# Performance work log

Measured on AMD Instinct MI355X. Metric: run time of the kernel, lower is better.

The kernel has to match this reference:

```python
import jax, jax.numpy as jnp
import numpy as np
from jax import lax

# ---- static config (matches init_kwargs) ----
BATCH, SEQ, D_MODEL = 2, 512, 1024
D_STATE, EXPAND, HEADDIM, D_CONV = 64, 2, 64, 4
VNUM, HORIZON = 3, 20
D_INNER = EXPAND * D_MODEL            # 2048
NHEADS = D_INNER // HEADDIM           # 32
CONV_DIM = D_INNER + 2 * D_STATE      # x, B, C go through the depthwise conv
D_IN_PROJ = 2 * D_INNER + 2 * D_STATE + NHEADS  # z | xBC | dt
RMS_EPS = 1e-5


def setup_inputs() -> dict:
    key = jax.random.key(0)
    ks = jax.random.split(key, 10)
    s = 0.02
    return {
        "embed_data": jax.random.normal(ks[0], (BATCH, SEQ, D_MODEL), jnp.float32),
        "in_proj_w": (jax.random.normal(ks[1], (D_IN_PROJ, D_MODEL), jnp.float32) * s),
        "conv_w": (jax.random.normal(ks[2], (CONV_DIM, D_CONV), jnp.float32) * s),
        "conv_b": jnp.zeros((CONV_DIM,), jnp.float32),
        # dt_bias = softplus^{-1}(dt_init) with dt_init ~ U(1e-3, 0.1), as in Mamba2
        "dt_bias": jnp.log(jnp.expm1(jax.random.uniform(ks[3], (NHEADS,), jnp.float32, 1e-3, 0.1))),
        # A = -exp(A_log), A_init ~ U(1, 16)
        "A_log": jnp.log(jax.random.uniform(ks[4], (NHEADS,), jnp.float32, 1.0, 16.0)),
        "D": jnp.ones((NHEADS,), jnp.float32),
        "norm_w": jnp.ones((D_INNER,), jnp.float32),
        "out_proj_w": (jax.random.normal(ks[5], (D_MODEL, D_INNER), jnp.float32) * s),
        "dec_cur_w": (jax.random.normal(ks[6], (VNUM, D_MODEL), jnp.float32) * s),
        "dec_cur_b": jnp.zeros((VNUM,), jnp.float32),
        "dec_fut_w": (jax.random.normal(ks[7], (HORIZON * VNUM, D_MODEL), jnp.float32) * s),
        "dec_fut_b": jnp.zeros((HORIZON * VNUM,), jnp.float32),
    }


def _mamba2(embed_data, in_proj_w, conv_w, conv_b, dt_bias, A_log, D, norm_w, out_proj_w):
    b, s, _ = embed_data.shape
    zxbcdt = jnp.einsum('bsd,ed->bse', embed_data, in_proj_w)  # [B,S,D_IN_PROJ]
    z = zxbcdt[..., :D_INNER]
    xBC = zxbcdt[..., D_INNER:D_INNER + CONV_DIM]
    dt = zxbcdt[..., D_INNER + CONV_DIM:]                      # [B,S,H]

    # causal depthwise conv1d (kernel=4) + silu
    xpad = jnp.pad(xBC, ((0, 0), (D_CONV - 1, 0), (0, 0)))
    xBC = sum(conv_w[:, k] * xpad[:, k:k + s, :] for k in range(D_CONV)) + conv_b
    xBC = jax.nn.silu(xBC)

    x = xBC[..., :D_INNER].reshape(b, s, NHEADS, HEADDIM)       # [B,S,H,P]
    Bm = xBC[..., D_INNER:D_INNER + D_STATE]                    # [B,S,N]
    Cm = xBC[..., D_INNER + D_STATE:]                           # [B,S,N]

    dt = jax.nn.softplus(dt + dt_bias)                          # [B,S,H]
    A = -jnp.exp(A_log)                                         # [H]

    # selective state-space scan: h_t = exp(dt*A) h_{t-1} + dt * x_t B_t^T
    def step(h, inp):
        x_t, dt_t, b_t, c_t = inp                               # [B,H,P],[B,H],[B,N],[B,N]
        dA = jnp.exp(dt_t * A)                                  # [B,H]
        h = h * dA[..., None, None] + (dt_t[..., None] * x_t)[..., None] * b_t[:, None, None, :]
        y = jnp.einsum('bhpn,bn->bhp', h, c_t)
        return h, y

    h0 = jnp.zeros((b, NHEADS, HEADDIM, D_STATE), embed_data.dtype)
    xs = (x.transpose(1, 0, 2, 3), dt.transpose(1, 0, 2),
          Bm.transpose(1, 0, 2), Cm.transpose(1, 0, 2))
    _, ys = lax.scan(step, h0, xs)                              # [S,B,H,P]
    y = ys.transpose(1, 0, 2, 3) + D[None, None, :, None] * x   # skip term D*x
    y = y.reshape(b, s, D_INNER)

    # gated RMSNorm: rmsnorm(y * silu(z)) * w
    y = y * jax.nn.silu(z)
    y = y * lax.rsqrt(jnp.mean(y * y, axis=-1, keepdims=True) + RMS_EPS) * norm_w
    return jnp.einsum('bsi,di->bsd', y, out_proj_w)             # [B,S,D_MODEL]


def reference(embed_data, in_proj_w, conv_w, conv_b, dt_bias, A_log, D, norm_w,
              out_proj_w, dec_cur_w, dec_cur_b, dec_fut_w, dec_fut_b):
    h = _mamba2(embed_data, in_proj_w, conv_w, conv_b, dt_bias, A_log, D, norm_w, out_proj_w)
    pred_current = jnp.einsum('bsd,vd->bsv', h, dec_cur_w) + dec_cur_b         # [B,S,V]
    pred_future = (h[:, -1] @ dec_fut_w.T + dec_fut_b).reshape(h.shape[0], HORIZON, VNUM)
    return (pred_current, pred_future)
```

## Files before the change

kernel.cpp:

```cpp
#include <hip/hip_runtime.h>
#include <hip/hip_bf16.h>

#define BATCH   2
#define SEQ     512
#define DMODEL  1024
#define DSTATE  64
#define HEADDIM 64
#define DCONV   4
#define VNUM    3
#define HORIZON 20
#define DINNER  2048
#define NHEADS  32
#define CONVDIM 2176
#define DINPROJ 4256
#define NPAD1   4352
#define BS      (BATCH*SEQ)
#define RMS_EPS 1e-5f
#define CHUNK   64
#define NCHUNK  (SEQ/CHUNK)
#define NDEC    (VNUM + HORIZON*VNUM)
#define WC_DS   32

typedef __attribute__((ext_vector_type(8))) short bf16x8;
typedef __attribute__((ext_vector_type(4))) float f32x4;

__device__ __forceinline__ unsigned short f2b(float x) {
    union { float f; unsigned u; } v; v.f = x;
    return (unsigned short)((v.u + 0x7fffu + ((v.u >> 16) & 1u)) >> 16);
}

__device__ __forceinline__ void async16(const void* g, const void* l) {
    __builtin_amdgcn_global_load_lds(
        (const __attribute__((address_space(1))) unsigned int*)g,
        (__attribute__((address_space(3))) unsigned int*)l, 16, 0, 0);
}

template<int BM, int BN, int FM, int FN, int KD>
__global__ __launch_bounds__(256) void gemm_bf16(const short* __restrict__ A,
                                                 const short* __restrict__ B,
                                                 float* __restrict__ C, int N) {
    constexpr int WM = FM * 16, WN = FN * 16;
    static_assert(BM == 2 * WM && BN == 2 * WN, "2x2 waves");
    __shared__ __align__(16) short At[BM * 32];
    __shared__ __align__(16) short Bt[BN * 32];
    const int t    = threadIdx.x;
    const int lane = t & 63;
    const int w    = t >> 6;
    const int wm   = (w >> 1) * WM, wn = (w & 1) * WN;
    const int row0 = blockIdx.y * BM, col0 = blockIdx.x * BN;
    const int fr   = lane & 15;
    const int kq   = lane >> 4;
    const int lr   = t >> 2;
    const int lc   = (t & 3) * 8;

    const short* Ag = A + (size_t)(row0 + lr) * KD + lc;
    const short* Bg = B + (size_t)(col0 + lr) * KD + lc;

    f32x4 acc[FM][FN];
#pragma unroll
    for (int i = 0; i < FM; ++i)
#pragma unroll
        for (int j = 0; j < FN; ++j)
#pragma unroll
            for (int r = 0; r < 4; ++r) acc[i][j][r] = 0.f;

    for (int k0 = 0; k0 < KD; k0 += 32) {
        __syncthreads();
#pragma unroll
        for (int i = 0; i < BM / 64; ++i)
            async16(Ag + (size_t)i * 64 * KD + k0, (const char*)At + i * 4096 + t * 16);
#pragma unroll
        for (int i = 0; i < BN / 64; ++i)
            async16(Bg + (size_t)i * 64 * KD + k0, (const char*)Bt + i * 4096 + t * 16);
        __syncthreads();

        bf16x8 af[FM], bv[FN];
#pragma unroll
        for (int i = 0; i < FM; ++i)
            af[i] = *(const bf16x8*)&At[(wm + i * 16 + fr) * 32 + kq * 8];
#pragma unroll
        for (int j = 0; j < FN; ++j)
            bv[j] = *(const bf16x8*)&Bt[(wn + j * 16 + fr) * 32 + kq * 8];
#pragma unroll
        for (int i = 0; i < FM; ++i)
#pragma unroll
            for (int j = 0; j < FN; ++j)
                acc[i][j] = __builtin_amdgcn_mfma_f32_16x16x32_bf16(
                    af[i], bv[j], acc[i][j], 0, 0, 0);
    }

    const int orow = lane >> 4;
#pragma unroll
    for (int i = 0; i < FM; ++i)
#pragma unroll
        for (int j = 0; j < FN; ++j) {
            const int col = col0 + wn + j * 16 + fr;
            if (col < N) {
#pragma unroll
                for (int r = 0; r < 4; ++r) {
                    const int row = row0 + wm + i * 16 + orow * 4 + r;
                    C[(size_t)row * N + col] = acc[i][j][r];
                }
            }
        }
}

#define EMB4  (BS * DMODEL / 4)
#define IPW4  (NPAD1 * DMODEL / 4)
__global__ __launch_bounds__(256) void cast_fused_kernel(
        const float* __restrict__ embed, const float* __restrict__ ipw,
        short* __restrict__ embB, short* __restrict__ ipwB) {
    const int i = blockIdx.x * 256 + threadIdx.x;
    if (i < EMB4) {
        float4 v = *(const float4*)(embed + (size_t)i * 4);
        *(short4*)(embB + (size_t)i * 4) =
            make_short4((short)f2b(v.x), (short)f2b(v.y),
                        (short)f2b(v.z), (short)f2b(v.w));
    } else {
        const int j = i - EMB4;
        const size_t e0 = (size_t)j * 4;
        const int row = (int)(e0 / DMODEL);
        short4 o;
        if (row < DINPROJ) {
            float4 v = *(const float4*)(ipw + e0);
            o = make_short4((short)f2b(v.x), (short)f2b(v.y),
                            (short)f2b(v.z), (short)f2b(v.w));
        } else {
            o = make_short4(0, 0, 0, 0);
        }
        *(short4*)(ipwB + e0) = o;
    }
}

__global__ __launch_bounds__(256) void wcomb_partial_kernel(
        const float* __restrict__ op, const float* __restrict__ cw,
        const float* __restrict__ fw, float* __restrict__ P) {
    const int itile = blockIdx.x & 7;
    const int ds    = blockIdx.x >> 3;
    const int i     = itile * 256 + threadIdx.x;
    const int d0    = ds * 32;

    __shared__ float lw[32][64];
#pragma unroll
    for (int k = 0; k < 8; ++k) {
        const int e = threadIdx.x * 8 + k;
        const int d = e >> 6, v = e & 63;
        float val = 0.f;
        if (v < VNUM)      val = cw[(size_t)v * DMODEL + d0 + d];
        else if (v < NDEC) val = fw[(size_t)(v - VNUM) * DMODEL + d0 + d];
        lw[d][v] = val;
    }

    float opc[32];
#pragma unroll
    for (int d = 0; d < 32; ++d) opc[d] = op[(size_t)(d0 + d) * DINNER + i];
    __syncthreads();

    f32x4 acc[16];
#pragma unroll
    for (int q = 0; q < 16; ++q)
#pragma unroll
        for (int r = 0; r < 4; ++r) acc[q][r] = 0.f;

#pragma unroll
    for (int d = 0; d < 32; ++d) {
        const float o = opc[d];
#pragma unroll
        for (int q = 0; q < 16; ++q) {
            float4 wv = *(const float4*)&lw[d][q * 4];
            acc[q][0] += o * wv.x; acc[q][1] += o * wv.y;
            acc[q][2] += o * wv.z; acc[q][3] += o * wv.w;
        }
    }

    float* Pp = P + (size_t)ds * 64 * DINNER + i;
#pragma unroll
    for (int q = 0; q < 16; ++q)
#pragma unroll
        for (int r = 0; r < 4; ++r)
            Pp[(size_t)(q * 4 + r) * DINNER] = acc[q][r];
}

__global__ __launch_bounds__(256) void wcomb_reduce_kernel(
        const float* __restrict__ P, float* __restrict__ W) {
    const int idx = blockIdx.x * 256 + threadIdx.x;
    float s = 0.f;
#pragma unroll
    for (int ds = 0; ds < WC_DS; ++ds) s += P[(size_t)ds * 64 * DINNER + idx];
    W[idx] = s;
}

#define CONVBLKS (BS * CONVDIM / 4 / 256)
__global__ __launch_bounds__(256) void conv_dt_kernel(
        const float* __restrict__ zxbcdt, const float* __restrict__ cw,
        const float* __restrict__ cb, const float* __restrict__ dt_bias,
        float* __restrict__ xbc, float* __restrict__ dts) {
    if (blockIdx.x < CONVBLKS) {
        const int item = blockIdx.x * 256 + threadIdx.x;
        const int c4 = item % (CONVDIM / 4);
        const int rs = item / (CONVDIM / 4);
        const int s  = rs % SEQ;
        const int c  = c4 * 4;
        const float* src = zxbcdt + (size_t)rs * DINPROJ + DINNER + c;
        float4 x0 = (s >= 3) ? *(const float4*)(src - 3 * DINPROJ) : make_float4(0,0,0,0);
        float4 x1 = (s >= 2) ? *(const float4*)(src - 2 * DINPROJ) : make_float4(0,0,0,0);
        float4 x2 = (s >= 1) ? *(const float4*)(src - 1 * DINPROJ) : make_float4(0,0,0,0);
        float4 x3 = *(const float4*)(src);
        float4 bias = *(const float4*)(cb + c);
        float4 r;
        {
            float4 w = *(const float4*)(cw + (size_t)(c+0)*4);
            r.x = bias.x + w.x*x0.x + w.y*x1.x + w.z*x2.x + w.w*x3.x;
        }
        {
            float4 w = *(const float4*)(cw + (size_t)(c+1)*4);
            r.y = bias.y + w.x*x0.y + w.y*x1.y + w.z*x2.y + w.w*x3.y;
        }
        {
            float4 w = *(const float4*)(cw + (size_t)(c+2)*4);
            r.z = bias.z + w.x*x0.z + w.y*x1.z + w.z*x2.z + w.w*x3.z;
        }
        {
            float4 w = *(const float4*)(cw + (size_t)(c+3)*4);
            r.w = bias.w + w.x*x0.w + w.y*x1.w + w.z*x2.w + w.w*x3.w;
        }
        r.x = r.x / (1.f + expf(-r.x));
        r.y = r.y / (1.f + expf(-r.y));
        r.z = r.z / (1.f + expf(-r.z));
        r.w = r.w / (1.f + expf(-r.w));
        *(float4*)(xbc + (size_t)rs * CONVDIM + c) = r;
    } else {
        const int idx = (blockIdx.x - CONVBLKS) * 256 + threadIdx.x;
        if (idx < BS * NHEADS) {
            const int h  = idx % NHEADS;
            const int rs = idx / NHEADS;
            const float v = zxbcdt[(size_t)rs * DINPROJ + DINNER + CONVDIM + h]
                            + dt_bias[h];
            dts[idx] = fmaxf(v, 0.f) + log1pf(expf(-fabsf(v)));
        }
    }
}

__global__ __launch_bounds__(256) void chunk_intra_kernel(
        const float* __restrict__ xbc, const float* __restrict__ dts,
        const float* __restrict__ A_log, const float* __restrict__ Dv,
        float* __restrict__ yraw, float* __restrict__ Sc,
        float* __restrict__ dexp) {
    const int blk = blockIdx.x;
    const int c  = blk & 7;
    const int bh = blk >> 3;
    const int h  = bh & 31;
    const int b  = bh >> 5;
    const int rs0 = b * SEQ + c * CHUNK;

    __shared__ float sBn[64][68];
    __shared__ float sX [64][68];
    __shared__ float sMT[64][68];
    __shared__ float sl[64], se[64], sdt[64];

    const int tid = threadIdx.x;
    const float A = -expf(A_log[h]);

    {
        const int row = tid >> 2;
        const int cq  = tid & 3;
        const float* xrow = xbc + (size_t)(rs0 + row) * CONVDIM;
#pragma unroll
        for (int i = 0; i < 4; ++i) {
            const int n = cq * 16 + i * 4;
            float4 bv = *(const float4*)(xrow + DINNER + n);
            float4 cv = *(const float4*)(xrow + DINNER + DSTATE + n);
            sBn[n+0][row] = bv.x; sBn[n+1][row] = bv.y;
            sBn[n+2][row] = bv.z; sBn[n+3][row] = bv.w;
            sX [n+0][row] = cv.x; sX [n+1][row] = cv.y;
            sX [n+2][row] = cv.z; sX [n+3][row] = cv.w;
        }
    }

    if (tid < 64) {
        const float dtv = dts[(size_t)(rs0 + tid) * NHEADS + h];
        sdt[tid] = dtv;
        float v = dtv * A;
#pragma unroll
        for (int off = 1; off < 64; off <<= 1) {
            float o = __shfl_up(v, off, 64);
            if (tid >= off) v += o;
        }
        sl[tid] = v;
        const float ltot = __shfl(v, 63, 64);
        se[tid] = expf(ltot - v);
        dexp[(size_t)blk * 64 + tid] = expf(v);
    }
    __syncthreads();

    const int g0 = (tid >> 4) * 4;
    const int g1 = (tid & 15) * 4;

    {
        const int t0 = g0, s0 = g1;
        float acc[4][4] = {};
        for (int n = 0; n < 64; ++n) {
            float4 ct = *(const float4*)&sX [n][t0];
            float4 bs = *(const float4*)&sBn[n][s0];
            float cta[4] = {ct.x, ct.y, ct.z, ct.w};
            float bsa[4] = {bs.x, bs.y, bs.z, bs.w};
#pragma unroll
            for (int i = 0; i < 4; ++i)
#pragma unroll
                for (int j = 0; j < 4; ++j) acc[i][j] += cta[i] * bsa[j];
        }
#pragma unroll
        for (int i = 0; i < 4; ++i) {
            const int t = t0 + i;
            const float lt = sl[t];
#pragma unroll
            for (int j = 0; j < 4; ++j) {
                const int s = s0 + j;
                sMT[s][t] = (s <= t) ? expf(lt - sl[s]) * acc[i][j] : 0.f;
            }
        }
    }
    __syncthreads();

    {
        const int row = tid >> 2;
        const int cq  = tid & 3;
        const float* xrow = xbc + (size_t)(rs0 + row) * CONVDIM + h * HEADDIM;
        const float dtv = sdt[row];
#pragma unroll
        for (int i = 0; i < 4; ++i) {
            const int p = cq * 16 + i * 4;
            float4 xv = *(const float4*)(xrow + p);
            sX[row][p+0] = dtv * xv.x; sX[row][p+1] = dtv * xv.y;
            sX[row][p+2] = dtv * xv.z; sX[row][p+3] = dtv * xv.w;
        }
    }
    __syncthreads();

    {
        const int t0 = g0, p0 = g1;
        float acc[4][4] = {};
        for (int s = 0; s < 64; ++s) {
            float4 mt = *(const float4*)&sMT[s][t0];
            float4 us = *(const float4*)&sX [s][p0];
            float mta[4] = {mt.x, mt.y, mt.z, mt.w};
            float usa[4] = {us.x, us.y, us.z, us.w};
#pragma unroll
            for (int i = 0; i < 4; ++i)
#pragma unroll
                for (int j = 0; j < 4; ++j) acc[i][j] += mta[i] * usa[j];
        }
        const float Dh = Dv[h];
#pragma unroll
        for (int i = 0; i < 4; ++i) {
            const int t = t0 + i;
            float4 xv = *(const float4*)(xbc + (size_t)(rs0 + t) * CONVDIM
                                         + h * HEADDIM + p0);
            float4 yv = make_float4(acc[i][0] + Dh * xv.x, acc[i][1] + Dh * xv.y,
                                    acc[i][2] + Dh * xv.z, acc[i][3] + Dh * xv.w);
            *(float4*)&yraw[(size_t)(rs0 + t) * DINNER + h * HEADDIM + p0] = yv;
        }
    }

    {
        const int p0 = g0, n0 = g1;
        float acc[4][4] = {};
        for (int s = 0; s < 64; ++s) {
            const float es = se[s];
            float4 up = *(const float4*)&sX[s][p0];
            float upa[4] = {es * up.x, es * up.y, es * up.z, es * up.w};
            float bna[4] = {sBn[n0+0][s], sBn[n0+1][s], sBn[n0+2][s], sBn[n0+3][s]};
#pragma unroll
            for (int i = 0; i < 4; ++i)
#pragma unroll
                for (int j = 0; j < 4; ++j) acc[i][j] += upa[i] * bna[j];
        }
        float* scp = Sc + (size_t)blk * (HEADDIM * DSTATE);
#pragma unroll
        for (int i = 0; i < 4; ++i) {
            float4 v = make_float4(acc[i][0], acc[i][1], acc[i][2], acc[i][3]);
            *(float4*)&scp[(size_t)(p0 + i) * DSTATE + n0] = v;
        }
    }
}

__global__ __launch_bounds__(256) void state_combine_kernel(
        const float* __restrict__ Sc, const float* __restrict__ dexp,
        float* __restrict__ h0ws) {
    const int bh  = blockIdx.x;
    const int tid = threadIdx.x;
    float hreg[16];
#pragma unroll
    for (int k = 0; k < 16; ++k) hreg[k] = 0.f;
    for (int c = 0; c < NCHUNK; ++c) {
        const size_t base = (size_t)(bh * NCHUNK + c) * (HEADDIM * DSTATE);
        const float ac = dexp[(size_t)(bh * NCHUNK + c) * 64 + 63];
#pragma unroll
        for (int k = 0; k < 16; ++k) {
            const int e = tid + k * 256;
            h0ws[base + e] = hreg[k];
            hreg[k] = ac * hreg[k] + Sc[base + e];
        }
    }
}

__global__ __launch_bounds__(256) void chunk_state_out_kernel(
        const float* __restrict__ xbc, const float* __restrict__ h0ws,
        const float* __restrict__ dexp, float* __restrict__ yraw) {
    const int blk = blockIdx.x;
    const int c  = blk & 7;
    if (c == 0) return;
    const int bh = blk >> 3;
    const int h  = bh & 31;
    const int b  = bh >> 5;
    const int rs0 = b * SEQ + c * CHUNK;

    __shared__ float sCn[64][68];
    __shared__ float sH [64][68];
    __shared__ float sdex[64];
    const int tid = threadIdx.x;
    {
        const int row = tid >> 2;
        const int cq  = tid & 3;
        const float* xrow = xbc + (size_t)(rs0 + row) * CONVDIM + DINNER + DSTATE;
        const float* hrow = h0ws + (size_t)blk * (HEADDIM * DSTATE) + (size_t)row * DSTATE;
#pragma unroll
        for (int i = 0; i < 4; ++i) {
            const int n = cq * 16 + i * 4;
            float4 cv = *(const float4*)(xrow + n);
            float4 hv = *(const float4*)(hrow + n);
            sCn[n+0][row] = cv.x; sCn[n+1][row] = cv.y;
            sCn[n+2][row] = cv.z; sCn[n+3][row] = cv.w;
            sH [n+0][row] = hv.x; sH [n+1][row] = hv.y;
            sH [n+2][row] = hv.z; sH [n+3][row] = hv.w;
        }
    }
    if (tid < 64) sdex[tid] = dexp[(size_t)blk * 64 + tid];
    __syncthreads();

    const int t0 = (tid >> 4) * 4;
    const int p0 = (tid & 15) * 4;
    float acc[4][4] = {};
    for (int n = 0; n < 64; ++n) {
        float4 ct = *(const float4*)&sCn[n][t0];
        float4 hp = *(const float4*)&sH [n][p0];
        float cta[4] = {ct.x, ct.y, ct.z, ct.w};
        float hpa[4] = {hp.x, hp.y, hp.z, hp.w};
#pragma unroll
        for (int i = 0; i < 4; ++i)
#pragma unroll
            for (int j = 0; j < 4; ++j) acc[i][j] += cta[i] * hpa[j];
    }
#pragma unroll
    for (int i = 0; i < 4; ++i) {
        const float d = sdex[t0 + i];
        float* yp = &yraw[(size_t)(rs0 + t0 + i) * DINNER + h * HEADDIM + p0];
        float4 old = *(const float4*)yp;
        *(float4*)yp = make_float4(old.x + d * acc[i][0], old.y + d * acc[i][1],
                                   old.z + d * acc[i][2], old.w + d * acc[i][3]);
    }
}

__global__ __launch_bounds__(256) void gate_norm_pred_kernel(
        const float* __restrict__ zxbcdt, const float* __restrict__ y,
        const float* __restrict__ nw, const float* __restrict__ W,
        const float* __restrict__ cur_b, float* __restrict__ out,
        float* __restrict__ ylast) {
    const int rs = blockIdx.x;
    const int t  = threadIdx.x;
    const float* z  = zxbcdt + (size_t)rs * DINPROJ;
    const float* yr = y + (size_t)rs * DINNER;

    float vals[8];
    float ss = 0.f;
#pragma unroll
    for (int i = 0; i < 8; ++i) {
        const int c = t + i * 256;
        const float zv = z[c];
        const float v  = yr[c] * (zv / (1.f + expf(-zv)));
        vals[i] = v;
        ss += v * v;
    }
#pragma unroll
    for (int off = 32; off > 0; off >>= 1) ss += __shfl_down(ss, off, 64);
    __shared__ float red[4];
    if ((t & 63) == 0) red[t >> 6] = ss;
    __syncthreads();
    const float tot   = red[0] + red[1] + red[2] + red[3];
    const float scale = rsqrtf(tot / (float)DINNER + RMS_EPS);

    const bool is_last = ((rs & (SEQ - 1)) == SEQ - 1);
    float p0 = 0.f, p1 = 0.f, p2 = 0.f;
#pragma unroll
    for (int i = 0; i < 8; ++i) {
        const int c = t + i * 256;
        const float vn = vals[i] * scale * nw[c];
        vals[i] = vn;
        p0 += vn * W[c];
        p1 += vn * W[DINNER + c];
        p2 += vn * W[2 * DINNER + c];
    }
    if (is_last) {
        float* yl = ylast + (size_t)(rs >> 9) * DINNER;
#pragma unroll
        for (int i = 0; i < 8; ++i) yl[t + i * 256] = vals[i];
    }
#pragma unroll
    for (int off = 32; off > 0; off >>= 1) {
        p0 += __shfl_down(p0, off, 64);
        p1 += __shfl_down(p1, off, 64);
        p2 += __shfl_down(p2, off, 64);
    }
    __shared__ float r3[4][3];
    if ((t & 63) == 0) { r3[t >> 6][0] = p0; r3[t >> 6][1] = p1; r3[t >> 6][2] = p2; }
    __syncthreads();
    if (t < VNUM) {
        const float s = r3[0][t] + r3[1][t] + r3[2][t] + r3[3][t];
        out[(size_t)rs * VNUM + t] = s + cur_b[t];
    }
}

__global__ __launch_bounds__(256) void pred_fut_kernel(
        const float* __restrict__ ylast, const float* __restrict__ W,
        const float* __restrict__ bvec, float* __restrict__ out) {
    const int blk = blockIdx.x;
    const int b = blk / (HORIZON * VNUM);
    const int j = blk % (HORIZON * VNUM);
    const float* yl = ylast + (size_t)b * DINNER;
    const float* wr = W + (size_t)(VNUM + j) * DINNER;
    float pv = 0.f;
    for (int i = threadIdx.x; i < DINNER; i += 256) pv += yl[i] * wr[i];
#pragma unroll
    for (int off = 32; off > 0; off >>= 1) pv += __shfl_down(pv, off, 64);
    __shared__ float red[4];
    if ((threadIdx.x & 63) == 0) red[threadIdx.x >> 6] = pv;
    __syncthreads();
    if (threadIdx.x == 0)
        out[b * (HORIZON * VNUM) + j] = red[0] + red[1] + red[2] + red[3] + bvec[j];
}

extern "C" void kernel_launch(void* const* d_in, const int* in_sizes, int n_in,
                              void* d_out, int out_size, void* d_ws, size_t ws_size,
                              hipStream_t stream) {
    const float* embed      = (const float*)d_in[0];
    const float* in_proj_w  = (const float*)d_in[1];
    const float* conv_w     = (const float*)d_in[2];
    const float* conv_b     = (const float*)d_in[3];
    const float* dt_bias    = (const float*)d_in[4];
    const float* A_log      = (const float*)d_in[5];
    const float* Dv         = (const float*)d_in[6];
    const float* norm_w     = (const float*)d_in[7];
    const float* out_proj_w = (const float*)d_in[8];
    const float* dec_cur_w  = (const float*)d_in[9];
    const float* dec_cur_b  = (const float*)d_in[10];
    const float* dec_fut_w  = (const float*)d_in[11];
    const float* dec_fut_b  = (const float*)d_in[12];

    float* ws     = (float*)d_ws;
    float* zxbcdt = ws;
    float* xbc    = zxbcdt + (size_t)BS * DINPROJ;
    float* dts    = xbc    + (size_t)BS * CONVDIM;
    float* yraw   = dts    + (size_t)BS * NHEADS;
    float* Sc     = yraw   + (size_t)BS * DINNER;
    float* h0ws   = Sc     + (size_t)BATCH*NHEADS*NCHUNK*HEADDIM*DSTATE;
    float* dexp   = h0ws   + (size_t)BATCH*NHEADS*NCHUNK*HEADDIM*DSTATE;
    float* Wp     = dexp   + (size_t)BATCH*NHEADS*NCHUNK*64;
    float* W      = Wp     + (size_t)WC_DS * 64 * DINNER;
    float* ylast  = W      + (size_t)64 * DINNER;
    short* embB   = (short*)(ylast + (size_t)BATCH * DINNER);
    short* ipwB   = embB + (size_t)BS * DMODEL;

    float* out = (float*)d_out;

    wcomb_partial_kernel<<<8 * WC_DS, 256, 0, stream>>>(out_proj_w, dec_cur_w,
                                                        dec_fut_w, Wp);
    wcomb_reduce_kernel<<<64 * DINNER / 256, 256, 0, stream>>>(Wp, W);

    cast_fused_kernel<<<(EMB4 + IPW4) / 256, 256, 0, stream>>>(embed, in_proj_w, embB, ipwB);
    gemm_bf16<128, 64, 4, 2, DMODEL>
        <<<dim3(NPAD1 / 64, BS / 128), 256, 0, stream>>>(embB, ipwB, zxbcdt, DINPROJ);

    conv_dt_kernel<<<CONVBLKS + (BS * NHEADS + 255) / 256, 256, 0, stream>>>(
        zxbcdt, conv_w, conv_b, dt_bias, xbc, dts);

    chunk_intra_kernel<<<BATCH * NHEADS * NCHUNK, 256, 0, stream>>>(
        xbc, dts, A_log, Dv, yraw, Sc, dexp);
    state_combine_kernel<<<BATCH * NHEADS, 256, 0, stream>>>(Sc, dexp, h0ws);
    chunk_state_out_kernel<<<BATCH * NHEADS * NCHUNK, 256, 0, stream>>>(
        xbc, h0ws, dexp, yraw);

    gate_norm_pred_kernel<<<BS, 256, 0, stream>>>(zxbcdt, yraw, norm_w, W,
                                                  dec_cur_b, out, ylast);

    pred_fut_kernel<<<BATCH * HORIZON * VNUM, 256, 0, stream>>>(ylast, W, dec_fut_b,
                                                                out + BS * VNUM);
}
```

Measured before the change: 186.9 us.

## Fuse conv and dt into chunk kernels and merge small preprocessing launches

The standalone conv/dt kernel and its xbc/dts intermediate buffers are removed. The chunk kernels now recompute the causal depthwise conv, SiLU and softplus directly from the in_proj output. The D skip term is rebuilt from the dt-scaled x kept in shared memory, by dividing by dt. The bf16 cast is merged with the wcomb partial kernel, and the wcomb reduce is merged with a state-combine pass that now splits work across 4x more blocks. This cuts launches and global traffic, at the cost of recomputing the B/C conv once per head and per chunk kernel.

```diff
diff --git a/kernel.cpp b/kernel.cpp
--- a/kernel.cpp
+++ b/kernel.cpp
@@ -29,6 +29,8 @@
     return (unsigned short)((v.u + 0x7fffu + ((v.u >> 16) & 1u)) >> 16);
 }
 
+__device__ __forceinline__ float silu(float x) { return x / (1.f + expf(-x)); }
+
 __device__ __forceinline__ void async16(const void* g, const void* l) {
     __builtin_amdgcn_global_load_lds(
         (const __attribute__((address_space(1))) unsigned int*)g,
@@ -105,49 +107,51 @@
         }
 }
 
-#define EMB4  (BS * DMODEL / 4)
-#define IPW4  (NPAD1 * DMODEL / 4)
-__global__ __launch_bounds__(256) void cast_fused_kernel(
+#define EMB4     (BS * DMODEL / 4)
+#define IPW4     (NPAD1 * DMODEL / 4)
+#define CASTBLKS ((EMB4 + IPW4) / 256)
+__global__ __launch_bounds__(256) void prep_kernel(
         const float* __restrict__ embed, const float* __restrict__ ipw,
-        short* __restrict__ embB, short* __restrict__ ipwB) {
-    const int i = blockIdx.x * 256 + threadIdx.x;
-    if (i < EMB4) {
-        float4 v = *(const float4*)(embed + (size_t)i * 4);
-        *(short4*)(embB + (size_t)i * 4) =
-            make_short4((short)f2b(v.x), (short)f2b(v.y),
-                        (short)f2b(v.z), (short)f2b(v.w));
-    } else {
-        const int j = i - EMB4;
-        const size_t e0 = (size_t)j * 4;
-        const int row = (int)(e0 / DMODEL);
-        short4 o;
-        if (row < DINPROJ) {
-            float4 v = *(const float4*)(ipw + e0);
-            o = make_short4((short)f2b(v.x), (short)f2b(v.y),
+        short* __restrict__ embB, short* __restrict__ ipwB,
+        const float* __restrict__ op, const float* __restrict__ cwv,
+        const float* __restrict__ fwv, float* __restrict__ P) {
+    __shared__ float lw[32][64];
+    if (blockIdx.x < CASTBLKS) {
+        const int i = blockIdx.x * 256 + threadIdx.x;
+        if (i < EMB4) {
+            float4 v = *(const float4*)(embed + (size_t)i * 4);
+            *(short4*)(embB + (size_t)i * 4) =
+                make_short4((short)f2b(v.x), (short)f2b(v.y),
                             (short)f2b(v.z), (short)f2b(v.w));
         } else {
-            o = make_short4(0, 0, 0, 0);
-        }
-        *(short4*)(ipwB + e0) = o;
-    }
-}
-
-__global__ __launch_bounds__(256) void wcomb_partial_kernel(
-        const float* __restrict__ op, const float* __restrict__ cw,
-        const float* __restrict__ fw, float* __restrict__ P) {
-    const int itile = blockIdx.x & 7;
-    const int ds    = blockIdx.x >> 3;
+            const int j = i - EMB4;
+            const size_t e0 = (size_t)j * 4;
+            const int row = (int)(e0 / DMODEL);
+            short4 o;
+            if (row < DINPROJ) {
+                float4 v = *(const float4*)(ipw + e0);
+                o = make_short4((short)f2b(v.x), (short)f2b(v.y),
+                                (short)f2b(v.z), (short)f2b(v.w));
+            } else {
+                o = make_short4(0, 0, 0, 0);
+            }
+            *(short4*)(ipwB + e0) = o;
+        }
+        return;
+    }
+    const int blk   = blockIdx.x - CASTBLKS;
+    const int itile = blk & 7;
+    const int ds    = blk >> 3;
     const int i     = itile * 256 + threadIdx.x;
     const int d0    = ds * 32;
 
-    __shared__ float lw[32][64];
 #pragma unroll
     for (int k = 0; k < 8; ++k) {
         const int e = threadIdx.x * 8 + k;
         const int d = e >> 6, v = e & 63;
         float val = 0.f;
-        if (v < VNUM)      val = cw[(size_t)v * DMODEL + d0 + d];
-        else if (v < NDEC) val = fw[(size_t)(v - VNUM) * DMODEL + d0 + d];
+        if (v < VNUM)      val = cwv[(size_t)v * DMODEL + d0 + d];
+        else if (v < NDEC) val = fwv[(size_t)(v - VNUM) * DMODEL + d0 + d];
         lw[d][v] = val;
     }
 
@@ -181,68 +185,9 @@
             Pp[(size_t)(q * 4 + r) * DINNER] = acc[q][r];
 }
 
-__global__ __launch_bounds__(256) void wcomb_reduce_kernel(
-        const float* __restrict__ P, float* __restrict__ W) {
-    const int idx = blockIdx.x * 256 + threadIdx.x;
-    float s = 0.f;
-#pragma unroll
-    for (int ds = 0; ds < WC_DS; ++ds) s += P[(size_t)ds * 64 * DINNER + idx];
-    W[idx] = s;
-}
-
-#define CONVBLKS (BS * CONVDIM / 4 / 256)
-__global__ __launch_bounds__(256) void conv_dt_kernel(
-        const float* __restrict__ zxbcdt, const float* __restrict__ cw,
+__global__ __launch_bounds__(256) void chunk_intra_kernel(
+        const float* __restrict__ zx, const float* __restrict__ cw,
         const float* __restrict__ cb, const float* __restrict__ dt_bias,
-        float* __restrict__ xbc, float* __restrict__ dts) {
-    if (blockIdx.x < CONVBLKS) {
-        const int item = blockIdx.x * 256 + threadIdx.x;
-        const int c4 = item % (CONVDIM / 4);
-        const int rs = item / (CONVDIM / 4);
-        const int s  = rs % SEQ;
-        const int c  = c4 * 4;
-        const float* src = zxbcdt + (size_t)rs * DINPROJ + DINNER + c;
-        float4 x0 = (s >= 3) ? *(const float4*)(src - 3 * DINPROJ) : make_float4(0,0,0,0);
-        float4 x1 = (s >= 2) ? *(const float4*)(src - 2 * DINPROJ) : make_float4(0,0,0,0);
-        float4 x2 = (s >= 1) ? *(const float4*)(src - 1 * DINPROJ) : make_float4(0,0,0,0);
-        float4 x3 = *(const float4*)(src);
-        float4 bias = *(const float4*)(cb + c);
-        float4 r;
-        {
-            float4 w = *(const float4*)(cw + (size_t)(c+0)*4);
-            r.x = bias.x + w.x*x0.x + w.y*x1.x + w.z*x2.x + w.w*x3.x;
-        }
-        {
-            float4 w = *(const float4*)(cw + (size_t)(c+1)*4);
-            r.y = bias.y + w.x*x0.y + w.y*x1.y + w.z*x2.y + w.w*x3.y;
-        }
-        {
-            float4 w = *(const float4*)(cw + (size_t)(c+2)*4);
-            r.z = bias.z + w.x*x0.z + w.y*x1.z + w.z*x2.z + w.w*x3.z;
-        }
-        {
-            float4 w = *(const float4*)(cw + (size_t)(c+3)*4);
-            r.w = bias.w + w.x*x0.w + w.y*x1.w + w.z*x2.w + w.w*x3.w;
-        }
-        r.x = r.x / (1.f + expf(-r.x));
-        r.y = r.y / (1.f + expf(-r.y));
-        r.z = r.z / (1.f + expf(-r.z));
-        r.w = r.w / (1.f + expf(-r.w));
-        *(float4*)(xbc + (size_t)rs * CONVDIM + c) = r;
-    } else {
-        const int idx = (blockIdx.x - CONVBLKS) * 256 + threadIdx.x;
-        if (idx < BS * NHEADS) {
-            const int h  = idx % NHEADS;
-            const int rs = idx / NHEADS;
-            const float v = zxbcdt[(size_t)rs * DINPROJ + DINNER + CONVDIM + h]
-                            + dt_bias[h];
-            dts[idx] = fmaxf(v, 0.f) + log1pf(expf(-fabsf(v)));
-        }
-    }
-}
-
-__global__ __launch_bounds__(256) void chunk_intra_kernel(
-        const float* __restrict__ xbc, const float* __restrict__ dts,
         const float* __restrict__ A_log, const float* __restrict__ Dv,
         float* __restrict__ yraw, float* __restrict__ Sc,
         float* __restrict__ dexp) {
@@ -261,24 +206,10 @@
     const int tid = threadIdx.x;
     const float A = -expf(A_log[h]);
 
-    {
-        const int row = tid >> 2;
-        const int cq  = tid & 3;
-        const float* xrow = xbc + (size_t)(rs0 + row) * CONVDIM;
-#pragma unroll
-        for (int i = 0; i < 4; ++i) {
-            const int n = cq * 16 + i * 4;
-            float4 bv = *(const float4*)(xrow + DINNER + n);
-            float4 cv = *(const float4*)(xrow + DINNER + DSTATE + n);
-            sBn[n+0][row] = bv.x; sBn[n+1][row] = bv.y;
-            sBn[n+2][row] = bv.z; sBn[n+3][row] = bv.w;
-            sX [n+0][row] = cv.x; sX [n+1][row] = cv.y;
-            sX [n+2][row] = cv.z; sX [n+3][row] = cv.w;
-        }
-    }
-
     if (tid < 64) {
-        const float dtv = dts[(size_t)(rs0 + tid) * NHEADS + h];
+        const float raw = zx[(size_t)(rs0 + tid) * DINPROJ + DINNER + CONVDIM + h]
+                          + dt_bias[h];
+        const float dtv = fmaxf(raw, 0.f) + log1pf(expf(-fabsf(raw)));
         sdt[tid] = dtv;
         float v = dtv * A;
 #pragma unroll
@@ -290,6 +221,42 @@
         const float ltot = __shfl(v, 63, 64);
         se[tid] = expf(ltot - v);
         dexp[(size_t)blk * 64 + tid] = expf(v);
+    }
+
+    {
+        const int row  = tid >> 2;
+        const int cq   = tid & 3;
+        const int spos = c * CHUNK + row;
+        const float* src = zx + (size_t)(rs0 + row) * DINPROJ + DINNER;
+#pragma unroll
+        for (int i = 0; i < 4; ++i) {
+            const int n = cq * 16 + i * 4;
+            float tB[4][4], tC[4][4];
+#pragma unroll
+            for (int j = 0; j < 4; ++j) {
+                if (spos >= 3 - j) {
+                    const float* tr = src + (ptrdiff_t)(j - 3) * DINPROJ;
+                    float4 bv = *(const float4*)(tr + 2048 + n);
+                    float4 cv = *(const float4*)(tr + 2112 + n);
+                    tB[j][0]=bv.x; tB[j][1]=bv.y; tB[j][2]=bv.z; tB[j][3]=bv.w;
+                    tC[j][0]=cv.x; tC[j][1]=cv.y; tC[j][2]=cv.z; tC[j][3]=cv.w;
+                } else {
+#pragma unroll
+                    for (int l = 0; l < 4; ++l) { tB[j][l] = 0.f; tC[j][l] = 0.f; }
+                }
+            }
+#pragma unroll
+            for (int l = 0; l < 4; ++l) {
+                float4 wB = *(const float4*)(cw + (size_t)(2048 + n + l) * 4);
+                float4 wC = *(const float4*)(cw + (size_t)(2112 + n + l) * 4);
+                float vB = cb[2048 + n + l] + wB.x * tB[0][l] + wB.y * tB[1][l]
+                           + wB.z * tB[2][l] + wB.w * tB[3][l];
+                float vC = cb[2112 + n + l] + wC.x * tC[0][l] + wC.y * tC[1][l]
+                           + wC.z * tC[2][l] + wC.w * tC[3][l];
+                sBn[n + l][row] = silu(vB);
+                sX [n + l][row] = silu(vC);
+            }
+        }
     }
     __syncthreads();
 
@@ -323,16 +290,32 @@
     __syncthreads();
 
     {
-        const int row = tid >> 2;
-        const int cq  = tid & 3;
-        const float* xrow = xbc + (size_t)(rs0 + row) * CONVDIM + h * HEADDIM;
+        const int row  = tid >> 2;
+        const int cq   = tid & 3;
+        const int spos = c * CHUNK + row;
         const float dtv = sdt[row];
+        const float* src = zx + (size_t)(rs0 + row) * DINPROJ + DINNER + h * HEADDIM;
 #pragma unroll
         for (int i = 0; i < 4; ++i) {
             const int p = cq * 16 + i * 4;
-            float4 xv = *(const float4*)(xrow + p);
-            sX[row][p+0] = dtv * xv.x; sX[row][p+1] = dtv * xv.y;
-            sX[row][p+2] = dtv * xv.z; sX[row][p+3] = dtv * xv.w;
+            float tx[4][4];
+#pragma unroll
+            for (int j = 0; j < 4; ++j) {
+                if (spos >= 3 - j) {
+                    float4 xv = *(const float4*)(src + (ptrdiff_t)(j - 3) * DINPROJ + p);
+                    tx[j][0]=xv.x; tx[j][1]=xv.y; tx[j][2]=xv.z; tx[j][3]=xv.w;
+                } else {
+#pragma unroll
+                    for (int l = 0; l < 4; ++l) tx[j][l] = 0.f;
+                }
+            }
+#pragma unroll
+            for (int l = 0; l < 4; ++l) {
+                float4 w = *(const float4*)(cw + (size_t)(h * HEADDIM + p + l) * 4);
+                float v = cb[h * HEADDIM + p + l] + w.x * tx[0][l] + w.y * tx[1][l]
+                          + w.z * tx[2][l] + w.w * tx[3][l];
+                sX[row][p + l] = dtv * silu(v);
+            }
         }
     }
     __syncthreads();
@@ -354,10 +337,10 @@
 #pragma unroll
         for (int i = 0; i < 4; ++i) {
             const int t = t0 + i;
-            float4 xv = *(const float4*)(xbc + (size_t)(rs0 + t) * CONVDIM
-                                         + h * HEADDIM + p0);
-            float4 yv = make_float4(acc[i][0] + Dh * xv.x, acc[i][1] + Dh * xv.y,
-                                    acc[i][2] + Dh * xv.z, acc[i][3] + Dh * xv.w);
+            const float dr = Dh / sdt[t];
+            float4 uv = *(const float4*)&sX[t][p0];
+            float4 yv = make_float4(acc[i][0] + dr * uv.x, acc[i][1] + dr * uv.y,
+                                    acc[i][2] + dr * uv.z, acc[i][3] + dr * uv.w);
             *(float4*)&yraw[(size_t)(rs0 + t) * DINNER + h * HEADDIM + p0] = yv;
         }
     }
@@ -384,28 +367,34 @@
     }
 }
 
-__global__ __launch_bounds__(256) void state_combine_kernel(
+__global__ __launch_bounds__(256) void comb_reduce_kernel(
         const float* __restrict__ Sc, const float* __restrict__ dexp,
-        float* __restrict__ h0ws) {
-    const int bh  = blockIdx.x;
-    const int tid = threadIdx.x;
-    float hreg[16];
-#pragma unroll
-    for (int k = 0; k < 16; ++k) hreg[k] = 0.f;
-    for (int c = 0; c < NCHUNK; ++c) {
-        const size_t base = (size_t)(bh * NCHUNK + c) * (HEADDIM * DSTATE);
-        const float ac = dexp[(size_t)(bh * NCHUNK + c) * 64 + 63];
-#pragma unroll
-        for (int k = 0; k < 16; ++k) {
-            const int e = tid + k * 256;
-            h0ws[base + e] = hreg[k];
-            hreg[k] = ac * hreg[k] + Sc[base + e];
-        }
+        float* __restrict__ h0ws, const float* __restrict__ P,
+        float* __restrict__ W) {
+    if (blockIdx.x < 256) {
+        const int bh = blockIdx.x >> 2;
+        const int e  = (blockIdx.x & 3) * 1024 + threadIdx.x * 4;
+        float4 h = make_float4(0.f, 0.f, 0.f, 0.f);
+        for (int c = 0; c < NCHUNK; ++c) {
+            const size_t base = (size_t)(bh * NCHUNK + c) * (HEADDIM * DSTATE);
+            const float ac = dexp[(size_t)(bh * NCHUNK + c) * 64 + 63];
+            *(float4*)&h0ws[base + e] = h;
+            float4 s = *(const float4*)&Sc[base + e];
+            h.x = ac * h.x + s.x; h.y = ac * h.y + s.y;
+            h.z = ac * h.z + s.z; h.w = ac * h.w + s.w;
+        }
+    } else {
+        const int idx = (blockIdx.x - 256) * 256 + threadIdx.x;
+        float s = 0.f;
+#pragma unroll
+        for (int ds = 0; ds < WC_DS; ++ds) s += P[(size_t)ds * 64 * DINNER + idx];
+        W[idx] = s;
     }
 }
 
 __global__ __launch_bounds__(256) void chunk_state_out_kernel(
-        const float* __restrict__ xbc, const float* __restrict__ h0ws,
+        const float* __restrict__ zx, const float* __restrict__ cw,
+        const float* __restrict__ cb, const float* __restrict__ h0ws,
         const float* __restrict__ dexp, float* __restrict__ yraw) {
     const int blk = blockIdx.x;
     const int c  = blk & 7;
@@ -422,17 +411,30 @@
     {
         const int row = tid >> 2;
         const int cq  = tid & 3;
-        const float* xrow = xbc + (size_t)(rs0 + row) * CONVDIM + DINNER + DSTATE;
-        const float* hrow = h0ws + (size_t)blk * (HEADDIM * DSTATE) + (size_t)row * DSTATE;
+        const float* src  = zx + (size_t)(rs0 + row) * DINPROJ + DINNER + 2112;
+        const float* hrow = h0ws + (size_t)blk * (HEADDIM * DSTATE)
+                            + (size_t)row * DSTATE;
 #pragma unroll
         for (int i = 0; i < 4; ++i) {
             const int n = cq * 16 + i * 4;
-            float4 cv = *(const float4*)(xrow + n);
+            float4 q0 = *(const float4*)(src - 3 * DINPROJ + n);
+            float4 q1 = *(const float4*)(src - 2 * DINPROJ + n);
+            float4 q2 = *(const float4*)(src - 1 * DINPROJ + n);
+            float4 q3 = *(const float4*)(src + n);
+            float t0a[4] = {q0.x, q0.y, q0.z, q0.w};
+            float t1a[4] = {q1.x, q1.y, q1.z, q1.w};
+            float t2a[4] = {q2.x, q2.y, q2.z, q2.w};
+            float t3a[4] = {q3.x, q3.y, q3.z, q3.w};
+#pragma unroll
+            for (int l = 0; l < 4; ++l) {
+                float4 w = *(const float4*)(cw + (size_t)(2112 + n + l) * 4);
+                float v = cb[2112 + n + l] + w.x * t0a[l] + w.y * t1a[l]
+                          + w.z * t2a[l] + w.w * t3a[l];
+                sCn[n + l][row] = silu(v);
+            }
             float4 hv = *(const float4*)(hrow + n);
-            sCn[n+0][row] = cv.x; sCn[n+1][row] = cv.y;
-            sCn[n+2][row] = cv.z; sCn[n+3][row] = cv.w;
-            sH [n+0][row] = hv.x; sH [n+1][row] = hv.y;
-            sH [n+2][row] = hv.z; sH [n+3][row] = hv.w;
+            sH[n+0][row] = hv.x; sH[n+1][row] = hv.y;
+            sH[n+2][row] = hv.z; sH[n+3][row] = hv.w;
         }
     }
     if (tid < 64) sdex[tid] = dexp[(size_t)blk * 64 + tid];
@@ -558,9 +560,7 @@
 
     float* ws     = (float*)d_ws;
     float* zxbcdt = ws;
-    float* xbc    = zxbcdt + (size_t)BS * DINPROJ;
-    float* dts    = xbc    + (size_t)BS * CONVDIM;
-    float* yraw   = dts    + (size_t)BS * NHEADS;
+    float* yraw   = zxbcdt + (size_t)BS * DINPROJ;
     float* Sc     = yraw   + (size_t)BS * DINNER;
     float* h0ws   = Sc     + (size_t)BATCH*NHEADS*NCHUNK*HEADDIM*DSTATE;
     float* dexp   = h0ws   + (size_t)BATCH*NHEADS*NCHUNK*HEADDIM*DSTATE;
@@ -572,22 +572,20 @@
 
     float* out = (float*)d_out;
 
-    wcomb_partial_kernel<<<8 * WC_DS, 256, 0, stream>>>(out_proj_w, dec_cur_w,
-                                                        dec_fut_w, Wp);
-    wcomb_reduce_kernel<<<64 * DINNER / 256, 256, 0, stream>>>(Wp, W);
-
-    cast_fused_kernel<<<(EMB4 + IPW4) / 256, 256, 0, stream>>>(embed, in_proj_w, embB, ipwB);
+    prep_kernel<<<CASTBLKS + 8 * WC_DS, 256, 0, stream>>>(
+        embed, in_proj_w, embB, ipwB, out_proj_w, dec_cur_w, dec_fut_w, Wp);
+
     gemm_bf16<128, 64, 4, 2, DMODEL>
         <<<dim3(NPAD1 / 64, BS / 128), 256, 0, stream>>>(embB, ipwB, zxbcdt, DINPROJ);
 
-    conv_dt_kernel<<<CONVBLKS + (BS * NHEADS + 255) / 256, 256, 0, stream>>>(
-        zxbcdt, conv_w, conv_b, dt_bias, xbc, dts);
-
     chunk_intra_kernel<<<BATCH * NHEADS * NCHUNK, 256, 0, stream>>>(
-        xbc, dts, A_log, Dv, yraw, Sc, dexp);
-    state_combine_kernel<<<BATCH * NHEADS, 256, 0, stream>>>(Sc, dexp, h0ws);
+        zxbcdt, conv_w, conv_b, dt_bias, A_log, Dv, yraw, Sc, dexp);
+
+    comb_reduce_kernel<<<256 + 64 * DINNER / 256, 256, 0, stream>>>(
+        Sc, dexp, h0ws, Wp, W);
+
     chunk_state_out_kernel<<<BATCH * NHEADS * NCHUNK, 256, 0, stream>>>(
-        xbc, h0ws, dexp, yraw);
+        zxbcdt, conv_w, conv_b, h0ws, dexp, yraw);
 
     gate_norm_pred_kernel<<<BS, 256, 0, stream>>>(zxbcdt, yraw, norm_w, W,
                                                   dec_cur_b, out, ylast);
```

Measured after the change: 196.4 us. +5.1%, slower.
